# Performance work log

Measured on AMD Instinct MI355X. Metric: run time of the kernel, lower is better.

The kernel has to match this reference:

```python
import jax, jax.numpy as jnp
import numpy as np

N = 40000          # nodes
E = 640000         # edges (avg degree 16)
D = 128            # in_channels == out_channels
G = 8              # graphs
NPG = N // G       # nodes per graph
EPS = 1e-6
SLOPE = 0.01       # torch LeakyReLU default


def leaky(x):
    return jnp.where(x >= 0, x, SLOPE * x)


def setup_inputs() -> dict:
    key = jax.random.key(0)
    ks = jax.random.split(key, 8)
    x = jax.random.normal(ks[0], (N, D), dtype=jnp.float32)
    edge_index = jax.random.randint(ks[1], (2, E), 0, N, dtype=jnp.int32)
    w = jax.random.uniform(ks[2], (E, 1), dtype=jnp.float32)
    batch = jnp.repeat(jnp.arange(G, dtype=jnp.int32), NPG)
    batch_num = jnp.full((G,), NPG, dtype=jnp.int32)
    s = 1.0 / np.sqrt(D)
    W1 = jax.random.uniform(ks[3], (D, D), jnp.float32, -s, s)
    W2 = jax.random.uniform(ks[4], (D, D), jnp.float32, -s, s)
    Wo = jax.random.uniform(ks[5], (D, D), jnp.float32, -s, s)
    Wn = jax.random.uniform(ks[6], (D, D), jnp.float32, -s, s)
    gamma = jnp.ones((D,), jnp.float32)
    beta = jnp.zeros((D,), jnp.float32)
    return {"x": x, "edge_index": edge_index, "w": w, "batch": batch,
            "batch_num": batch_num, "W1": W1, "W2": W2, "Wo": Wo, "Wn": Wn,
            "gamma": gamma, "beta": beta}


def reference(x, edge_index, w, batch, batch_num, W1, W2, Wo, Wn, gamma, beta):
    # mlp_x (dropout in eval mode => identity)
    h = leaky(x @ W1) @ W2                                    # [N, D]
    # gather -> scale -> scatter-sum -> activate
    xj = w * h[edge_index[1]]                                 # [E, D]
    xn = leaky(jax.ops.segment_sum(xj, edge_index[0], num_segments=N))
    out = h @ Wo + xn @ Wn                                    # [N, D]
    # GraphNorm: per-graph mean and unbiased std (torch_scatter defaults)
    cnt = batch_num.astype(jnp.float32)[:, None]              # [G, 1]
    mu = jax.ops.segment_sum(out, batch, num_segments=G) / cnt
    diff = out - mu[batch]
    var = jax.ops.segment_sum(diff * diff, batch, num_segments=G) / (cnt - 1.0)
    sigma = jnp.sqrt(var)
    return diff / (sigma[batch] + EPS) * gamma + beta
```

## Files before the change

kernel.cpp:

```cpp
#include <hip/hip_runtime.h>
#include <hip/hip_bf16.h>

#define D 128
#define NN 40000
#define EE 640000
#define GG 8
#define NPG 5000
#define CAP 32
#define OVCAP 4096

using short8 = __attribute__((ext_vector_type(8))) short;
using f32x4 = __attribute__((ext_vector_type(4))) float;

__device__ __forceinline__ float lrelu(float v) { return v >= 0.f ? v : 0.01f * v; }

__device__ __forceinline__ ushort f2bf(float f) {
    union { float f; uint u; } c; c.f = f;
    return (ushort)((c.u + 0x7FFFu + ((c.u >> 16) & 1u)) >> 16);
}
__device__ __forceinline__ float bf2f_lo(uint u) { union { uint u; float f; } c; c.u = u << 16; return c.f; }
__device__ __forceinline__ float bf2f_hi(uint u) { union { uint u; float f; } c; c.u = u & 0xFFFF0000u; return c.f; }

__global__ __launch_bounds__(256) void wtrans_k(const float* __restrict__ W1,
                                                const float* __restrict__ W2,
                                                const float* __restrict__ Wo,
                                                const float* __restrict__ Wn,
                                                short* __restrict__ WT) {
    const float* W = blockIdx.x == 0 ? W1 : blockIdx.x == 1 ? W2 : blockIdx.x == 2 ? Wo : Wn;
    short* T = WT + blockIdx.x * (D * D);
#pragma unroll 4
    for (int i = 0; i < 64; ++i) {
        int flat = threadIdx.x + i * 256;
        int k = flat >> 7, n = flat & 127;
        T[n * D + k] = (short)f2bf(W[flat]);
    }
}

template <int ABF, int LKA>
__device__ __forceinline__ void mm_pass(const void* __restrict__ Av,
                                        const short* __restrict__ WT,
                                        short (*As)[136], short (*Bs)[136],
                                        f32x4 (&acc)[8], int arow, int tid) {
    const uint4* bsrc = (const uint4*)WT;
#pragma unroll
    for (int i = 0; i < 8; ++i) {
        int idx = tid + i * 256;
        int flat = idx * 8;
        *(uint4*)&Bs[flat >> 7][flat & 127] = bsrc[idx];
    }
    if constexpr (ABF) {
        const uint4* asrc = (const uint4*)Av;
#pragma unroll
        for (int i = 0; i < 4; ++i) {
            int idx = tid + i * 256;
            int flat = idx * 8;
            *(uint4*)&As[flat >> 7][flat & 127] = asrc[(size_t)arow * 16 + idx];
        }
    } else {
        const float4* A4 = (const float4*)Av;
#pragma unroll
        for (int i = 0; i < 8; ++i) {
            int idx = tid + i * 256;
            int row = idx >> 5, kq = idx & 31;
            float4 v = A4[(size_t)(arow + row) * 32 + kq];
            if (LKA) { v.x = lrelu(v.x); v.y = lrelu(v.y); v.z = lrelu(v.z); v.w = lrelu(v.w); }
            uint2 p;
            p.x = (uint)f2bf(v.x) | ((uint)f2bf(v.y) << 16);
            p.y = (uint)f2bf(v.z) | ((uint)f2bf(v.w) << 16);
            *(uint2*)&As[row][kq * 4] = p;
        }
    }
    __syncthreads();
    const int lane = tid & 63;
    const int m0 = (tid >> 6) * 16;
    const int lrow = lane & 15;
    const int kgrp = (lane >> 4) * 8;
#pragma unroll
    for (int ks = 0; ks < 4; ++ks) {
        const int kb = ks * 32 + kgrp;
        short8 a = *(const short8*)&As[m0 + lrow][kb];
#pragma unroll
        for (int nt = 0; nt < 8; ++nt) {
            short8 b = *(const short8*)&Bs[nt * 16 + lrow][kb];
            acc[nt] = __builtin_amdgcn_mfma_f32_16x16x32_bf16(a, b, acc[nt], 0, 0, 0);
        }
    }
    __syncthreads();
}

template <int A1BF, int LK1, int TWO, int A2BF, int LK2, int LKOUT, int CBF>
__global__ __launch_bounds__(256) void mm_k(const void* __restrict__ A1,
                                            const short* __restrict__ WT1,
                                            const void* __restrict__ A2,
                                            const short* __restrict__ WT2,
                                            void* __restrict__ Cv) {
    __shared__ short As[64][136];
    __shared__ short Bs[128][136];
    const int tid = threadIdx.x;
    const int arow = blockIdx.x * 64;
    f32x4 acc[8] = {};
    mm_pass<A1BF, LK1>(A1, WT1, As, Bs, acc, arow, tid);
    if constexpr (TWO) mm_pass<A2BF, LK2>(A2, WT2, As, Bs, acc, arow, tid);

    const int lane = tid & 63;
    const int c0 = lane & 15;
    const int r0 = (tid >> 6) * 16 + ((lane >> 4) << 2);
#pragma unroll
    for (int nt = 0; nt < 8; ++nt) {
#pragma unroll
        for (int r = 0; r < 4; ++r) {
            float v = acc[nt][r];
            if (LKOUT) v = lrelu(v);
            const size_t off = (size_t)(arow + r0 + r) * D + nt * 16 + c0;
            if constexpr (CBF) ((ushort*)Cv)[off] = f2bf(v);
            else ((float*)Cv)[off] = v;
        }
    }
}

__global__ __launch_bounds__(256) void fill_k(const int* __restrict__ ei,
                                              const float* __restrict__ w,
                                              int* __restrict__ deg,
                                              int* __restrict__ csr_src,
                                              float* __restrict__ csr_w,
                                              int* __restrict__ ov) {
    const int e = blockIdx.x * 256 + threadIdx.x;
    const int dst = ei[e];
    const int src = ei[EE + e];
    const float we = w[e];
    const int pos = atomicAdd(&deg[dst], 1);
    if (pos < CAP) {
        csr_src[dst * CAP + pos] = src;
        csr_w[dst * CAP + pos] = we;
    } else {
        const int oi = atomicAdd(&ov[0], 1);
        if (oi < OVCAP) ov[1 + oi] = e;
    }
}

__global__ __launch_bounds__(256) void gather_k(const ushort* __restrict__ h,
                                                const int* __restrict__ deg,
                                                const int* __restrict__ csr_src,
                                                const float* __restrict__ csr_w,
                                                float* __restrict__ xn) {
    const int n = blockIdx.x * 4 + (threadIdx.x >> 6);
    const int lane = threadIdx.x & 63;
    int dn = deg[n];
    if (dn > CAP) dn = CAP;
    float2 acc = {0.f, 0.f};
#pragma unroll 2
    for (int j = 0; j < dn; ++j) {
        const int src = csr_src[n * CAP + j];
        const float wv = csr_w[n * CAP + j];
        const uint v = *((const uint*)(h + (size_t)src * D) + lane);
        acc.x += wv * bf2f_lo(v);
        acc.y += wv * bf2f_hi(v);
    }
    *((float2*)(xn + (size_t)n * D) + lane) = acc;
}

__global__ __launch_bounds__(256) void overflow_k(const ushort* __restrict__ h,
                                                  const int* __restrict__ ei,
                                                  const float* __restrict__ w,
                                                  const int* __restrict__ ov,
                                                  float* __restrict__ xn) {
    int cnt = ov[0];
    if (cnt > OVCAP) cnt = OVCAP;
    const int wid = threadIdx.x >> 6;
    const int lane = threadIdx.x & 63;
    for (int i = wid; i < cnt; i += 4) {
        const int e = ov[1 + i];
        const int dst = ei[e];
        const int src = ei[EE + e];
        const float we = w[e];
        const uint v = *((const uint*)(h + (size_t)src * D) + lane);
        float* xr = xn + (size_t)dst * D + lane * 2;
        atomicAdd(xr, bf2f_lo(v) * we);
        atomicAdd(xr + 1, bf2f_hi(v) * we);
    }
}

__global__ __launch_bounds__(256) void stats_k(const float* __restrict__ out,
                                               float* __restrict__ stats) {
    const int g = blockIdx.x / 50, chunk = blockIdx.x % 50;
    const int d = threadIdx.x & 127, half = threadIdx.x >> 7;
    size_t base = ((size_t)g * NPG + chunk * 100) * D + d;
    float s = 0.f, ss = 0.f;
#pragma unroll 4
    for (int r = half; r < 100; r += 2) {
        float v = out[base + (size_t)r * D];
        s += v; ss += v * v;
    }
    atomicAdd(&stats[g * D + d], s);
    atomicAdd(&stats[GG * D + g * D + d], ss);
}

__global__ __launch_bounds__(256) void norm_k(float* __restrict__ out,
                                              const float* __restrict__ stats,
                                              const float* __restrict__ gamma,
                                              const float* __restrict__ beta) {
    const int i4 = blockIdx.x * 256 + threadIdx.x;
    const int row = i4 >> 5;
    const int g = row / NPG;
    const int d0 = (i4 & 31) * 4;
    float4 v = *((float4*)out + i4);
    const float4 s4 = *(const float4*)&stats[g * D + d0];
    const float4 q4 = *(const float4*)&stats[GG * D + g * D + d0];
    const float4 g4 = *(const float4*)&gamma[d0];
    const float4 b4 = *(const float4*)&beta[d0];
    const float inv = 1.f / (float)NPG;
    const float invm1 = 1.f / (float)(NPG - 1);
    float mu, var, sg;
    mu = s4.x * inv; var = (q4.x - s4.x * mu) * invm1; sg = sqrtf(fmaxf(var, 0.f));
    v.x = (v.x - mu) / (sg + 1e-6f) * g4.x + b4.x;
    mu = s4.y * inv; var = (q4.y - s4.y * mu) * invm1; sg = sqrtf(fmaxf(var, 0.f));
    v.y = (v.y - mu) / (sg + 1e-6f) * g4.y + b4.y;
    mu = s4.z * inv; var = (q4.z - s4.z * mu) * invm1; sg = sqrtf(fmaxf(var, 0.f));
    v.z = (v.z - mu) / (sg + 1e-6f) * g4.z + b4.z;
    mu = s4.w * inv; var = (q4.w - s4.w * mu) * invm1; sg = sqrtf(fmaxf(var, 0.f));
    v.w = (v.w - mu) / (sg + 1e-6f) * g4.w + b4.w;
    *((float4*)out + i4) = v;
}

extern "C" void kernel_launch(void* const* d_in, const int* in_sizes, int n_in,
                              void* d_out, int out_size, void* d_ws, size_t ws_size,
                              hipStream_t stream) {
    const float* x = (const float*)d_in[0];
    const int* ei = (const int*)d_in[1];
    const float* w = (const float*)d_in[2];
    const float* W1 = (const float*)d_in[5];
    const float* W2 = (const float*)d_in[6];
    const float* Wo = (const float*)d_in[7];
    const float* Wn = (const float*)d_in[8];
    const float* gamma = (const float*)d_in[9];
    const float* beta = (const float*)d_in[10];
    float* out = (float*)d_out;

    char* ws = (char*)d_ws;
    const size_t BF16MAT = (size_t)NN * D * 2;
    const size_t F32MAT = (size_t)NN * D * 4;
    size_t off = 0;
    ushort* t1 = (ushort*)(ws + off);  off += BF16MAT;
    ushort* h = (ushort*)(ws + off);   off += BF16MAT;
    float* xn = (float*)(ws + off);    off += F32MAT;
    float* stats = (float*)(ws + off); off += 2 * GG * D * 4 + 256;
    short* WT = (short*)(ws + off);    off += 4 * (size_t)D * D * 2;
    int* deg = (int*)(ws + off);       off += (size_t)NN * 4;
    int* ov = (int*)(ws + off);        off += (1 + OVCAP) * 4 + 252; off &= ~(size_t)255;
    int* csr_src = (int*)(ws + off);   off += (size_t)NN * CAP * 4;
    float* csr_w = (float*)(ws + off);

    const int MM_GRID = NN / 64;

    wtrans_k<<<4, 256, 0, stream>>>(W1, W2, Wo, Wn, WT);
    mm_k<0, 0, 0, 0, 0, 1, 1><<<MM_GRID, 256, 0, stream>>>(x, WT, x, WT, t1);
    mm_k<1, 0, 0, 1, 0, 0, 1><<<MM_GRID, 256, 0, stream>>>(t1, WT + D * D, t1, WT + D * D, h);
    hipMemsetAsync(deg, 0, (size_t)NN * 4, stream);
    hipMemsetAsync(ov, 0, (1 + OVCAP) * 4, stream);
    hipMemsetAsync(stats, 0, 2 * GG * D * 4, stream);
    fill_k<<<EE / 256, 256, 0, stream>>>(ei, w, deg, csr_src, csr_w, ov);
    gather_k<<<NN / 4, 256, 0, stream>>>(h, deg, csr_src, csr_w, xn);
    overflow_k<<<1, 256, 0, stream>>>(h, ei, w, ov, xn);
    mm_k<1, 0, 1, 0, 1, 0, 0><<<MM_GRID, 256, 0, stream>>>(h, WT + 2 * D * D, xn, WT + 3 * D * D, out);
    stats_k<<<GG * 50, 256, 0, stream>>>(out, stats);
    norm_k<<<(NN * D / 4) / 256, 256, 0, stream>>>(out, stats, gamma, beta);
}
```

Baseline: 230.8 us.

## Fuse two MLP matmuls into one kernel, pack CSR pairs, batch gather loads

The two MLP matmuls are merged into a single kernel that keeps the leaky-ReLU intermediate in shared memory, so the bf16 t1 buffer is never written to or read back from global memory and one launch is removed. The CSR source index and edge weight are packed into one int2 array, so each edge needs one load instead of two. The gather loop is unrolled into batches of 8 and 4 with independent row loads, giving more memory-level parallelism on the random row reads. The cost is higher register pressure in the gather kernel and more code.

```diff
diff --git a/kernel.cpp b/kernel.cpp
--- a/kernel.cpp
+++ b/kernel.cpp
@@ -36,11 +36,8 @@
     }
 }
 
-template <int ABF, int LKA>
-__device__ __forceinline__ void mm_pass(const void* __restrict__ Av,
-                                        const short* __restrict__ WT,
-                                        short (*As)[136], short (*Bs)[136],
-                                        f32x4 (&acc)[8], int arow, int tid) {
+__device__ __forceinline__ void stage_B(const short* __restrict__ WT,
+                                        short (*Bs)[136], int tid) {
     const uint4* bsrc = (const uint4*)WT;
 #pragma unroll
     for (int i = 0; i < 8; ++i) {
@@ -48,6 +45,11 @@
         int flat = idx * 8;
         *(uint4*)&Bs[flat >> 7][flat & 127] = bsrc[idx];
     }
+}
+
+template <int ABF, int LKA>
+__device__ __forceinline__ void stage_A(const void* __restrict__ Av,
+                                        short (*As)[136], int arow, int tid) {
     if constexpr (ABF) {
         const uint4* asrc = (const uint4*)Av;
 #pragma unroll
@@ -70,7 +72,10 @@
             *(uint2*)&As[row][kq * 4] = p;
         }
     }
-    __syncthreads();
+}
+
+__device__ __forceinline__ void do_mfma(short (*As)[136], short (*Bs)[136],
+                                        f32x4 (&acc)[8], int tid) {
     const int lane = tid & 63;
     const int m0 = (tid >> 6) * 16;
     const int lrow = lane & 15;
@@ -85,7 +90,40 @@
             acc[nt] = __builtin_amdgcn_mfma_f32_16x16x32_bf16(a, b, acc[nt], 0, 0, 0);
         }
     }
-    __syncthreads();
+}
+
+__global__ __launch_bounds__(256) void mlp_k(const float* __restrict__ x,
+                                             const short* __restrict__ W1T,
+                                             const short* __restrict__ W2T,
+                                             ushort* __restrict__ h) {
+    __shared__ short As[64][136];
+    __shared__ short Bs[128][136];
+    const int tid = threadIdx.x;
+    const int arow = blockIdx.x * 64;
+    f32x4 acc[8] = {};
+    stage_A<0, 0>(x, As, arow, tid);
+    stage_B(W1T, Bs, tid);
+    __syncthreads();
+    do_mfma(As, Bs, acc, tid);
+    __syncthreads();
+    const int lane = tid & 63;
+    const int c0 = lane & 15;
+    const int r0 = (tid >> 6) * 16 + ((lane >> 4) << 2);
+#pragma unroll
+    for (int nt = 0; nt < 8; ++nt)
+#pragma unroll
+        for (int r = 0; r < 4; ++r)
+            As[r0 + r][nt * 16 + c0] = (short)f2bf(lrelu(acc[nt][r]));
+    stage_B(W2T, Bs, tid);
+#pragma unroll
+    for (int nt = 0; nt < 8; ++nt) acc[nt] = f32x4{0.f, 0.f, 0.f, 0.f};
+    __syncthreads();
+    do_mfma(As, Bs, acc, tid);
+#pragma unroll
+    for (int nt = 0; nt < 8; ++nt)
+#pragma unroll
+        for (int r = 0; r < 4; ++r)
+            h[(size_t)(arow + r0 + r) * D + nt * 16 + c0] = f2bf(acc[nt][r]);
 }
 
 template <int A1BF, int LK1, int TWO, int A2BF, int LK2, int LKOUT, int CBF>
@@ -99,9 +137,18 @@
     const int tid = threadIdx.x;
     const int arow = blockIdx.x * 64;
     f32x4 acc[8] = {};
-    mm_pass<A1BF, LK1>(A1, WT1, As, Bs, acc, arow, tid);
-    if constexpr (TWO) mm_pass<A2BF, LK2>(A2, WT2, As, Bs, acc, arow, tid);
-
+    stage_A<A1BF, LK1>(A1, As, arow, tid);
+    stage_B(WT1, Bs, tid);
+    __syncthreads();
+    do_mfma(As, Bs, acc, tid);
+    __syncthreads();
+    if constexpr (TWO) {
+        stage_A<A2BF, LK2>(A2, As, arow, tid);
+        stage_B(WT2, Bs, tid);
+        __syncthreads();
+        do_mfma(As, Bs, acc, tid);
+        __syncthreads();
+    }
     const int lane = tid & 63;
     const int c0 = lane & 15;
     const int r0 = (tid >> 6) * 16 + ((lane >> 4) << 2);
@@ -121,8 +168,7 @@
 __global__ __launch_bounds__(256) void fill_k(const int* __restrict__ ei,
                                               const float* __restrict__ w,
                                               int* __restrict__ deg,
-                                              int* __restrict__ csr_src,
-                                              float* __restrict__ csr_w,
+                                              int2* __restrict__ csr,
                                               int* __restrict__ ov) {
     const int e = blockIdx.x * 256 + threadIdx.x;
     const int dst = ei[e];
@@ -130,8 +176,7 @@
     const float we = w[e];
     const int pos = atomicAdd(&deg[dst], 1);
     if (pos < CAP) {
-        csr_src[dst * CAP + pos] = src;
-        csr_w[dst * CAP + pos] = we;
+        csr[dst * CAP + pos] = make_int2(src, __float_as_int(we));
     } else {
         const int oi = atomicAdd(&ov[0], 1);
         if (oi < OVCAP) ov[1 + oi] = e;
@@ -140,19 +185,46 @@
 
 __global__ __launch_bounds__(256) void gather_k(const ushort* __restrict__ h,
                                                 const int* __restrict__ deg,
-                                                const int* __restrict__ csr_src,
-                                                const float* __restrict__ csr_w,
+                                                const int2* __restrict__ csr,
                                                 float* __restrict__ xn) {
     const int n = blockIdx.x * 4 + (threadIdx.x >> 6);
     const int lane = threadIdx.x & 63;
     int dn = deg[n];
     if (dn > CAP) dn = CAP;
+    const int2* row = csr + (size_t)n * CAP;
     float2 acc = {0.f, 0.f};
-#pragma unroll 2
-    for (int j = 0; j < dn; ++j) {
-        const int src = csr_src[n * CAP + j];
-        const float wv = csr_w[n * CAP + j];
-        const uint v = *((const uint*)(h + (size_t)src * D) + lane);
+    int j = 0;
+    for (; j + 8 <= dn; j += 8) {
+        int2 p[8]; uint v[8];
+#pragma unroll
+        for (int t = 0; t < 8; ++t) p[t] = row[j + t];
+#pragma unroll
+        for (int t = 0; t < 8; ++t) v[t] = *((const uint*)(h + (size_t)p[t].x * D) + lane);
+#pragma unroll
+        for (int t = 0; t < 8; ++t) {
+            const float wv = __int_as_float(p[t].y);
+            acc.x += wv * bf2f_lo(v[t]);
+            acc.y += wv * bf2f_hi(v[t]);
+        }
+    }
+    if (j + 4 <= dn) {
+        int2 p[4]; uint v[4];
+#pragma unroll
+        for (int t = 0; t < 4; ++t) p[t] = row[j + t];
+#pragma unroll
+        for (int t = 0; t < 4; ++t) v[t] = *((const uint*)(h + (size_t)p[t].x * D) + lane);
+#pragma unroll
+        for (int t = 0; t < 4; ++t) {
+            const float wv = __int_as_float(p[t].y);
+            acc.x += wv * bf2f_lo(v[t]);
+            acc.y += wv * bf2f_hi(v[t]);
+        }
+        j += 4;
+    }
+    for (; j < dn; ++j) {
+        int2 p = row[j];
+        const uint v = *((const uint*)(h + (size_t)p.x * D) + lane);
+        const float wv = __int_as_float(p.y);
         acc.x += wv * bf2f_lo(v);
         acc.y += wv * bf2f_hi(v);
     }
@@ -240,26 +312,23 @@
     const size_t BF16MAT = (size_t)NN * D * 2;
     const size_t F32MAT = (size_t)NN * D * 4;
     size_t off = 0;
-    ushort* t1 = (ushort*)(ws + off);  off += BF16MAT;
     ushort* h = (ushort*)(ws + off);   off += BF16MAT;
     float* xn = (float*)(ws + off);    off += F32MAT;
     float* stats = (float*)(ws + off); off += 2 * GG * D * 4 + 256;
     short* WT = (short*)(ws + off);    off += 4 * (size_t)D * D * 2;
     int* deg = (int*)(ws + off);       off += (size_t)NN * 4;
     int* ov = (int*)(ws + off);        off += (1 + OVCAP) * 4 + 252; off &= ~(size_t)255;
-    int* csr_src = (int*)(ws + off);   off += (size_t)NN * CAP * 4;
-    float* csr_w = (float*)(ws + off);
+    int2* csr = (int2*)(ws + off);
 
     const int MM_GRID = NN / 64;
 
     wtrans_k<<<4, 256, 0, stream>>>(W1, W2, Wo, Wn, WT);
-    mm_k<0, 0, 0, 0, 0, 1, 1><<<MM_GRID, 256, 0, stream>>>(x, WT, x, WT, t1);
-    mm_k<1, 0, 0, 1, 0, 0, 1><<<MM_GRID, 256, 0, stream>>>(t1, WT + D * D, t1, WT + D * D, h);
+    mlp_k<<<MM_GRID, 256, 0, stream>>>(x, WT, WT + D * D, h);
     hipMemsetAsync(deg, 0, (size_t)NN * 4, stream);
     hipMemsetAsync(ov, 0, (1 + OVCAP) * 4, stream);
     hipMemsetAsync(stats, 0, 2 * GG * D * 4, stream);
-    fill_k<<<EE / 256, 256, 0, stream>>>(ei, w, deg, csr_src, csr_w, ov);
-    gather_k<<<NN / 4, 256, 0, stream>>>(h, deg, csr_src, csr_w, xn);
+    fill_k<<<EE / 256, 256, 0, stream>>>(ei, w, deg, csr, ov);
+    gather_k<<<NN / 4, 256, 0, stream>>>(h, deg, csr, xn);
     overflow_k<<<1, 256, 0, stream>>>(h, ei, w, ov, xn);
     mm_k<1, 0, 1, 0, 1, 0, 0><<<MM_GRID, 256, 0, stream>>>(h, WT + 2 * D * D, xn, WT + 3 * D * D, out);
     stats_k<<<GG * 50, 256, 0, stream>>>(out, stats);
```

After: 217.9 us. 5.6% less time.
